# Kernel optimization log

Hardware: AMD Instinct MI355X
Metric: run time of the kernel (lower is better)

## Reference

```python
import jax, jax.numpy as jnp
import numpy as np

N = 50000
E = 800000
F_IN = 128
HID = 16
HEADS = 8
C = 16
NEG_SLOPE = 0.2


def setup_inputs() -> dict:
    key = jax.random.key(0)
    ks = jax.random.split(key, 12)
    glorot = lambda k, shape: jax.random.normal(k, shape, jnp.float32) * jnp.sqrt(2.0 / (shape[0] + shape[-1]))
    return {
        "x": jax.random.normal(ks[0], (N, F_IN), jnp.float32),
        "edge_index": jax.random.randint(ks[1], (2, E), 0, N, jnp.int32),
        "x2": jax.random.normal(ks[2], (N, F_IN), jnp.float32),
        "edge_index2": jax.random.randint(ks[3], (2, E), 0, N, jnp.int32),
        # conv1: GATConv(F_IN -> HID, heads=HEADS, concat=True)
        "W1": glorot(ks[4], (F_IN, HEADS * HID)),
        "a1_src": glorot(ks[5], (HEADS, HID)),
        "a1_dst": glorot(ks[6], (HEADS, HID)),
        "b1": jnp.zeros((HEADS * HID,), jnp.float32),
        # conv2: GATConv(HEADS*HID -> C, heads=1, concat=False)
        "W2": glorot(ks[7], (HEADS * HID, 1 * C)),
        "a2_src": glorot(ks[8], (1, C)),
        "a2_dst": glorot(ks[9], (1, C)),
        "b2": jnp.zeros((C,), jnp.float32),
    }


def gat_conv(x, edge_index, W, a_src, a_dst, bias, concat):
    """PyG-style GATConv with self-loops, segment softmax over destinations."""
    n = x.shape[0]
    heads, out = a_src.shape
    h = (x @ W).reshape(n, heads, out)               # [N, H, O]
    loops = jnp.arange(n, dtype=edge_index.dtype)
    src = jnp.concatenate([edge_index[0], loops])     # messages flow src -> dst
    dst = jnp.concatenate([edge_index[1], loops])
    alpha_s = jnp.einsum('nho,ho->nh', h, a_src)
    alpha_d = jnp.einsum('nho,ho->nh', h, a_dst)
    e = jax.nn.leaky_relu(alpha_s[src] + alpha_d[dst], NEG_SLOPE)  # [E+N, H]
    m = jax.lax.stop_gradient(jax.ops.segment_max(e, dst, num_segments=n))
    w = jnp.exp(e - m[dst])
    denom = jax.ops.segment_sum(w, dst, num_segments=n)
    alpha = w / (denom[dst] + 1e-16)                  # segment softmax
    msg = h[src] * alpha[:, :, None]                  # [E+N, H, O]
    agg = jax.ops.segment_sum(msg, dst, num_segments=n)
    agg = agg.reshape(n, heads * out) if concat else agg.mean(axis=1)
    return agg + bias


def forward_once(x, edge_index, W1, a1_src, a1_dst, b1, W2, a2_src, a2_dst, b2):
    # dropout(p=0.6) is identity in eval mode
    h = jax.nn.elu(gat_conv(x, edge_index, W1, a1_src, a1_dst, b1, concat=True))
    return gat_conv(h, edge_index, W2, a2_src, a2_dst, b2, concat=False)


def reference(x, edge_index, x2, edge_index2, W1, a1_src, a1_dst, b1, W2, a2_src, a2_dst, b2):
    y = forward_once(x, edge_index, W1, a1_src, a1_dst, b1, W2, a2_src, a2_dst, b2)
    z = forward_once(x2, edge_index2, W1, a1_src, a1_dst, b1, W2, a2_src, a2_dst, b2)
    eps = 1e-8
    ny = jnp.maximum(jnp.linalg.norm(y, axis=1), eps)
    nz = jnp.maximum(jnp.linalg.norm(z, axis=1), eps)
    cos = jnp.sum(y * z, axis=1) / (ny * nz)
    ls_y = jax.nn.log_softmax(y, axis=1)
    ls_z = jax.nn.log_softmax(z, axis=1)
    return (ls_y, 1.0 - cos, ls_z, ls_y, ls_y)
```

## Files before the change

kernel.cpp:

```cpp
#include <hip/hip_runtime.h>
#include <hip/hip_bf16.h>

#define N_NODES 50000
#define N_EDGES 800000
#define F_INS   128
#define HIDDEN  16
#define HEADS   8
#define HO      128
#define C_OUT   16
#define NEG_SLOPE 0.2f
#define SLOT    64
#define NB_G1   ((N_NODES + 63) / 64)
#define NB_GAT1 ((N_NODES + 3) / 4)
#define NB_G2   ((N_NODES + 16) / 16)

#define NP      50016
#define AS_ST   ((size_t)NP * 8)
#define H1B_ST  ((size_t)NP * 64)
#define HL1_ST  ((size_t)N_NODES * 64)
#define H2_ST   ((size_t)NP * 16)
#define AS2_ST  ((size_t)NP)

#define NCLS     128
#define CLS_MUL  1342u
#define CLS_SH   19
#define CAP      8192
#define CHUNK    2048
#define NB_BKT   ((N_EDGES + CHUNK - 1) / CHUNK)

typedef unsigned short u16;
typedef unsigned int   u32;
typedef int v4i __attribute__((ext_vector_type(4)));
typedef short bf16x8 __attribute__((ext_vector_type(8)));
typedef float f32x4 __attribute__((ext_vector_type(4)));

__device__ __forceinline__ float bf2f(u16 u) {
    union { u32 i; float f; } t; t.i = ((u32)u) << 16; return t.f;
}
__device__ __forceinline__ float bflo(u32 q) {
    union { u32 i; float f; } t; t.i = q << 16; return t.f;
}
__device__ __forceinline__ float bfhi(u32 q) {
    union { u32 i; float f; } t; t.i = q & 0xFFFF0000u; return t.f;
}
__device__ __forceinline__ u32 f2bf(float f) {
    union { float f; u32 i; } t; t.f = f;
    u32 x = t.i;
    u32 lsb = (x >> 16) & 1u;
    x += 0x7FFFu + lsb;
    return x >> 16;
}
__device__ __forceinline__ float lrelu(float t) {
    return fmaxf(t, NEG_SLOPE * t);
}
__device__ __forceinline__ int cls_of(int d) { return (int)(((u32)d * CLS_MUL) >> CLS_SH); }
__host__ __device__ __forceinline__ int cls_base(int c) { return (int)(((u32)c * 524288u + (CLS_MUL - 1)) / CLS_MUL); }

__global__ void k_wt(const float* __restrict__ W1, const float* __restrict__ a1s,
                     const float* __restrict__ a1d, u32* __restrict__ w1t,
                     u32* __restrict__ a1t) {
    int t = threadIdx.x;
    if (blockIdx.x < 32) {
        int e = blockIdx.x * 256 + t;
        int c = e >> 6, kp = e & 63;
        float lo = W1[(2 * kp) * 128 + c];
        float hi = W1[(2 * kp + 1) * 128 + c];
        w1t[e] = (f2bf(hi) << 16) | f2bf(lo);
    } else {
        #pragma unroll
        for (int i = 0; i < 4; ++i) {
            int wi = t + i * 256;
            int n = wi >> 6, kp = wi & 63;
            int h = n >> 1;
            const float* av = ((n & 1) ? a1d : a1s) + h * 16;
            float s0 = 0.f, s1 = 0.f;
            #pragma unroll
            for (int c = 0; c < 16; ++c) {
                s0 += W1[(2 * kp) * 128 + h * 16 + c] * av[c];
                s1 += W1[(2 * kp + 1) * 128 + h * 16 + c] * av[c];
            }
            a1t[wi] = (f2bf(s1) << 16) | f2bf(s0);
        }
    }
}

__launch_bounds__(256)
__global__ void k_bucket(const int* __restrict__ ei0, const int* __restrict__ ei1,
                         int* __restrict__ gcur, u32* __restrict__ bucket) {
    __shared__ int cnt[NCLS];
    __shared__ int base[NCLS];
    int t = threadIdx.x;
    int g = blockIdx.x & 1;
    int chunk = blockIdx.x >> 1;
    int e0 = chunk * CHUNK + t * 8;
    bool act = e0 < N_EDGES;

    if (t < NCLS) cnt[t] = 0;
    __syncthreads();

    const int* src = g ? ei1 : ei0;
    const int* dst = src + N_EDGES;
    int d8[8], s8[8], c8[8];
    if (act) {
        v4i da = *(const v4i*)(dst + e0), db = *(const v4i*)(dst + e0 + 4);
        v4i sa = *(const v4i*)(src + e0), sb = *(const v4i*)(src + e0 + 4);
        d8[0]=da[0]; d8[1]=da[1]; d8[2]=da[2]; d8[3]=da[3];
        d8[4]=db[0]; d8[5]=db[1]; d8[6]=db[2]; d8[7]=db[3];
        s8[0]=sa[0]; s8[1]=sa[1]; s8[2]=sa[2]; s8[3]=sa[3];
        s8[4]=sb[0]; s8[5]=sb[1]; s8[6]=sb[2]; s8[7]=sb[3];
        #pragma unroll
        for (int j = 0; j < 8; ++j) {
            c8[j] = cls_of(d8[j]);
            atomicAdd(&cnt[c8[j]], 1);
        }
    }
    __syncthreads();
    if (t < NCLS) {
        int n = cnt[t];
        base[t] = n ? atomicAdd(&gcur[g * NCLS + t], n) : 0;
        cnt[t] = 0;
    }
    __syncthreads();
    if (act) {
        #pragma unroll
        for (int j = 0; j < 8; ++j) {
            int c = c8[j];
            int p = atomicAdd(&cnt[c], 1);
            bucket[(size_t)(g * NCLS + c) * CAP + base[c] + p] =
                ((u32)d8[j] << 16) | (u32)s8[j];
        }
    }
}

__launch_bounds__(256)
__global__ void k_build(const int* __restrict__ gcur, const u32* __restrict__ bucket,
                        int* __restrict__ cursor, u16* __restrict__ col) {
    __shared__ int cnt[391];
    int t = threadIdx.x;
    int c = blockIdx.x & (NCLS - 1);
    int g = blockIdx.x >> 7;
    int d0 = cls_base(c);
    int d1 = (c == NCLS - 1) ? N_NODES : cls_base(c + 1);
    int nn = d1 - d0;
    for (int j = t; j < nn; j += 256) cnt[j] = 0;
    __syncthreads();

    int size = gcur[g * NCLS + c];
    const u32* bp = bucket + (size_t)(g * NCLS + c) * CAP;
    u16* cl = col + (size_t)g * N_NODES * SLOT;
    for (int i = t; i < size; i += 256) {
        u32 e = bp[i];
        int d = (int)(e >> 16);
        int s = (int)(e & 0xFFFFu);
        int p = atomicAdd(&cnt[d - d0], 1);
        if (p < SLOT) cl[(size_t)d * SLOT + p] = (u16)s;
    }
    __syncthreads();
    int* cur = cursor + g * N_NODES;
    for (int j = t; j < nn; j += 256) {
        int d = d0 + j;
        int raw = cnt[j];
        int n0 = min(raw, SLOT);
        int n1 = (n0 + 7) & ~7;
        u16* cw = cl + (size_t)d * SLOT;
        for (int p = n0; p < n1; ++p) cw[p] = (u16)N_NODES;
        cur[d] = raw;
    }
}

__launch_bounds__(256)
__global__ void k_gemm1(const float* __restrict__ x1g, const float* __restrict__ x2g,
                        const u32* __restrict__ w1t, const u32* __restrict__ a1t,
                        u32* __restrict__ h1b, float* __restrict__ as_,
                        float* __restrict__ ad_) {
    __shared__ u32 xls[4096];
    int t = threadIdx.x;
    int bid = blockIdx.x;
    int g = bid >= NB_G1;
    if (g) bid -= NB_G1;
    const float* x = g ? x2g : x1g;
    u32*   h1o = h1b + (size_t)g * H1B_ST;
    float* aso = as_ + (size_t)g * AS_ST;
    float* ado = ad_ + (size_t)g * AS_ST;
    int r0 = bid * 64;

    const float2* x2p = (const float2*)x;
    #pragma unroll
    for (int i = 0; i < 16; ++i) {
        int A = t + i * 256;
        int wi = A >> 10, kt = (A >> 8) & 3, L = (A >> 2) & 63, jj = A & 3;
        int m = L & 15, qd = L >> 4;
        int r = r0 + wi * 16 + m;
        int pp = kt * 16 + qd * 4 + jj;
        float2 v = make_float2(0.f, 0.f);
        if (r < N_NODES) v = x2p[(size_t)r * 64 + pp];
        xls[A] = (f2bf(v.y) << 16) | f2bf(v.x);
    }
    __syncthreads();

    int lane = t & 63;
    int wid = t >> 6;
    int n = lane & 15, quad = lane >> 4;

    f32x4 acc[8], acca;
    #pragma unroll
    for (int ct = 0; ct < 8; ++ct) acc[ct] = (f32x4){0.f, 0.f, 0.f, 0.f};
    acca = (f32x4){0.f, 0.f, 0.f, 0.f};

    #pragma unroll
    for (int kt = 0; kt < 4; ++kt) {
        union { uint4 u; bf16x8 v; } af;
        af.u = *(const uint4*)(xls + wid * 1024 + kt * 256 + lane * 4);
        #pragma unroll
        for (int ct = 0; ct < 8; ++ct) {
            union { uint4 u; bf16x8 v; } bf_;
            bf_.u = *(const uint4*)(w1t + (ct * 16 + n) * 64 + kt * 16 + quad * 4);
            acc[ct] = __builtin_amdgcn_mfma_f32_16x16x32_bf16(af.v, bf_.v, acc[ct], 0, 0, 0);
        }
        union { uint4 u; bf16x8 v; } ba;
        ba.u = *(const uint4*)(a1t + n * 64 + kt * 16 + quad * 4);
        acca = __builtin_amdgcn_mfma_f32_16x16x32_bf16(af.v, ba.v, acca, 0, 0, 0);
    }

    int h = n >> 1;
    #pragma unroll
    for (int reg = 0; reg < 4; ++reg) {
        int gr = r0 + wid * 16 + quad * 4 + reg;
        bool ok = gr <= N_NODES;
        float av = (gr == N_NODES) ? -1e30f : acca[reg];
        if (ok) {
            if (n & 1) ado[gr * 8 + h] = av;
            else       aso[gr * 8 + h] = av;
        }
        #pragma unroll
        for (int ct = 0; ct < 8; ++ct) {
            u32 my = f2bf(acc[ct][reg]);
            u32 ot = (u32)__shfl_xor((int)my, 1);
            if (!(n & 1) && ok)
                h1o[(size_t)gr * 64 + ct * 8 + (n >> 1)] = (ot << 16) | my;
        }
    }
}

__launch_bounds__(256)
__global__ void k_gat1(const u32* __restrict__ h1b, const float* __restrict__ as_,
                       const float* __restrict__ ad_, const int* __restrict__ cursor,
                       const u16* __restrict__ col, const float* __restrict__ b1,
                       u32* __restrict__ hL1) {
    int t = threadIdx.x;
    int lane = t & 63;
    int bid = blockIdx.x;
    int g = bid >= NB_GAT1;
    if (g) bid -= NB_GAT1;
    int node = bid * 4 + (t >> 6);

    const u32*   h1  = h1b + (size_t)g * H1B_ST;
    const float* as1 = as_ + (size_t)g * AS_ST;
    const float* ad1 = ad_ + (size_t)g * AS_ST;
    const u16*   cp  = col + ((size_t)g * N_NODES + node) * SLOT;

    int hc = lane >> 3;
    int ha = lane & 7;
    int j8 = lane >> 3;
    int vb = hc << 2;

    float ad_a = ad1[node * 8 + ha];
    float as_c = as1[node * 8 + hc];
    float ad_c = ad1[node * 8 + hc];

    float w = __expf(lrelu(as_c + ad_c));
    float denom = w;
    u32 q = h1[(u32)node * 64 + (u32)lane];
    float ax = w * bflo(q), ay = w * bfhi(q);

    int deg = min(cursor[g * N_NODES + node], SLOT);
    int nb = (deg + 7) >> 3;
    for (int b = 0; b < nb; ++b) {
        int e = b * 8;
        ushort4 sa4 = *(const ushort4*)(cp + e);
        ushort4 sb4 = *(const ushort4*)(cp + e + 4);
        u32 q0 = h1[((u32)sa4.x << 6) | (u32)lane];
        u32 q1 = h1[((u32)sa4.y << 6) | (u32)lane];
        u32 q2 = h1[((u32)sa4.z << 6) | (u32)lane];
        u32 q3 = h1[((u32)sa4.w << 6) | (u32)lane];
        u32 q4 = h1[((u32)sb4.x << 6) | (u32)lane];
        u32 q5 = h1[((u32)sb4.y << 6) | (u32)lane];
        u32 q6 = h1[((u32)sb4.z << 6) | (u32)lane];
        u32 q7 = h1[((u32)sb4.w << 6) | (u32)lane];

        int sA = cp[e + j8];
        float A = as1[sA * 8 + ha];
        int wli = __float_as_int(__expf(lrelu(A + ad_a)));
        float w0 = __int_as_float(__builtin_amdgcn_ds_bpermute(vb,       wli));
        float w1 = __int_as_float(__builtin_amdgcn_ds_bpermute(vb + 32,  wli));
        float w2 = __int_as_float(__builtin_amdgcn_ds_bpermute(vb + 64,  wli));
        float w3 = __int_as_float(__builtin_amdgcn_ds_bpermute(vb + 96,  wli));
        float w4 = __int_as_float(__builtin_amdgcn_ds_bpermute(vb + 128, wli));
        float w5 = __int_as_float(__builtin_amdgcn_ds_bpermute(vb + 160, wli));
        float w6 = __int_as_float(__builtin_amdgcn_ds_bpermute(vb + 192, wli));
        float w7 = __int_as_float(__builtin_amdgcn_ds_bpermute(vb + 224, wli));

        denom += ((w0 + w1) + (w2 + w3)) + ((w4 + w5) + (w6 + w7));
        ax += w0 * bflo(q0) + w1 * bflo(q1) + w2 * bflo(q2) + w3 * bflo(q3)
            + w4 * bflo(q4) + w5 * bflo(q5) + w6 * bflo(q6) + w7 * bflo(q7);
        ay += w0 * bfhi(q0) + w1 * bfhi(q1) + w2 * bfhi(q2) + w3 * bfhi(q3)
            + w4 * bfhi(q4) + w5 * bfhi(q5) + w6 * bfhi(q6) + w7 * bfhi(q7);
    }
    float inv = 1.f / (denom + 1e-16f);
    int c = lane * 2;
    float o0 = ax * inv + b1[c];
    float o1 = ay * inv + b1[c + 1];
    o0 = (o0 > 0.f) ? o0 : (__expf(o0) - 1.f);
    o1 = (o1 > 0.f) ? o1 : (__expf(o1) - 1.f);
    hL1[(size_t)g * HL1_ST + (size_t)node * 64 + lane] = (f2bf(o1) << 16) | f2bf(o0);
}

__launch_bounds__(256)
__global__ void k_gemm2(const u32* __restrict__ hL1, const float* __restrict__ W2,
                        const float* __restrict__ a2s, const float* __restrict__ a2d,
                        float* __restrict__ h2, float* __restrict__ as2,
                        float* __restrict__ ad2) {
    __shared__ float w2s[F_INS * C_OUT];
    __shared__ float hs[16 * 136];
    int t = threadIdx.x;
    int bid = blockIdx.x;
    int g = bid >= NB_G2;
    if (g) bid -= NB_G2;
    const u16* hL = (const u16*)(hL1 + (size_t)g * HL1_ST);
    float* h2o  = h2  + (size_t)g * H2_ST;
    float* as2o = as2 + (size_t)g * AS2_ST;
    float* ad2o = ad2 + (size_t)g * AS2_ST;

    const float4* w4 = (const float4*)W2;
    #pragma unroll
    for (int i = 0; i < 2; ++i) {
        int idx = t + i * 256;
        ((float4*)w2s)[idx] = w4[idx];
    }
    int r0 = bid * 16;
    const ushort4* hg = (const ushort4*)hL;
    #pragma unroll
    for (int i = 0; i < 2; ++i) {
        int idx = t + i * 256;
        int r  = idx >> 5;
        int c4 = idx & 31;
        ushort4 qq = make_ushort4(0, 0, 0, 0);
        if (r0 + r < N_NODES) qq = hg[(size_t)(r0 + r) * 32 + c4];
        float4 v; v.x = bf2f(qq.x); v.y = bf2f(qq.y); v.z = bf2f(qq.z); v.w = bf2f(qq.w);
        *(float4*)(hs + r * 136 + c4 * 4) = v;
    }
    __syncthreads();

    int c = t & 15, r = t >> 4;
    float acc = 0.f;
    #pragma unroll 8
    for (int k = 0; k < F_INS; ++k) acc += hs[r * 136 + k] * w2s[k * C_OUT + c];
    int n = r0 + r;
    if (n <= N_NODES) h2o[(size_t)n * C_OUT + c] = acc;

    float sa = acc * a2s[c];
    float sd = acc * a2d[c];
    #pragma unroll
    for (int m = 1; m < 16; m <<= 1) {
        sa += __shfl_xor(sa, m);
        sd += __shfl_xor(sd, m);
    }
    if (c == 0 && n <= N_NODES) {
        as2o[n] = (n == N_NODES) ? -1e30f : sa;
        ad2o[n] = sd;
    }
}

__device__ __forceinline__ float gat2_node(const float* __restrict__ h2g,
                                           const float* __restrict__ as2g,
                                           const float* __restrict__ ad2g,
                                           const int* __restrict__ curg,
                                           const u16* __restrict__ cp,
                                           const float* __restrict__ b2,
                                           int node, int c) {
    float ad = ad2g[node];
    float w = __expf(lrelu(as2g[node] + ad));
    float denom = w;
    float acc = w * h2g[(u32)node * C_OUT + (u32)c];

    int deg = min(curg[node], SLOT);
    int nb = (deg + 7) >> 3;
    for (int b = 0; b < nb; ++b) {
        const u16* ce = cp + b * 8;
        ushort4 sa4 = *(const ushort4*)ce;
        ushort4 sb4 = *(const ushort4*)(ce + 4);
        int s0 = sa4.x, s1 = sa4.y, s2 = sa4.z, s3 = sa4.w;
        int s4 = sb4.x, s5 = sb4.y, s6 = sb4.z, s7 = sb4.w;
        float A0 = as2g[s0], A1 = as2g[s1], A2 = as2g[s2], A3 = as2g[s3];
        float A4 = as2g[s4], A5 = as2g[s5], A6 = as2g[s6], A7 = as2g[s7];
        float v0 = h2g[(u32)(s0 * C_OUT + c)], v1 = h2g[(u32)(s1 * C_OUT + c)];
        float v2 = h2g[(u32)(s2 * C_OUT + c)], v3 = h2g[(u32)(s3 * C_OUT + c)];
        float v4 = h2g[(u32)(s4 * C_OUT + c)], v5 = h2g[(u32)(s5 * C_OUT + c)];
        float v6 = h2g[(u32)(s6 * C_OUT + c)], v7 = h2g[(u32)(s7 * C_OUT + c)];
        float w0 = __expf(lrelu(A0 + ad)), w1 = __expf(lrelu(A1 + ad));
        float w2 = __expf(lrelu(A2 + ad)), w3 = __expf(lrelu(A3 + ad));
        float w4 = __expf(lrelu(A4 + ad)), w5 = __expf(lrelu(A5 + ad));
        float w6 = __expf(lrelu(A6 + ad)), w7 = __expf(lrelu(A7 + ad));
        denom += ((w0 + w1) + (w2 + w3)) + ((w4 + w5) + (w6 + w7));
        acc += (w0 * v0 + w1 * v1 + w2 * v2 + w3 * v3)
             + (w4 * v4 + w5 * v5 + w6 * v6 + w7 * v7);
    }
    return acc / (denom + 1e-16f) + b2[c];
}

__launch_bounds__(256)
__global__ void k_gat2e(const float* __restrict__ h2, const float* __restrict__ as2,
                        const float* __restrict__ ad2, const int* __restrict__ cursor,
                        const u16* __restrict__ col, const float* __restrict__ b2,
                        float* __restrict__ out) {
    int t = threadIdx.x;
    int node = blockIdx.x * 16 + (t >> 4);
    int c = t & 15;

    float yv = gat2_node(h2, as2, ad2, cursor,
                         col + (size_t)node * SLOT, b2, node, c);
    float zv = gat2_node(h2 + H2_ST, as2 + AS2_ST, ad2 + AS2_ST, cursor + N_NODES,
                         col + ((size_t)N_NODES + node) * SLOT, b2, node, c);

    float my = yv, mz = zv;
    #pragma unroll
    for (int m = 1; m < 16; m <<= 1) {
        my = fmaxf(my, __shfl_xor(my, m));
        mz = fmaxf(mz, __shfl_xor(mz, m));
    }
    float sy = __expf(yv - my), sz = __expf(zv - mz);
    float dot = yv * zv, ny = yv * yv, nz = zv * zv;
    #pragma unroll
    for (int m = 1; m < 16; m <<= 1) {
        sy  += __shfl_xor(sy, m);
        sz  += __shfl_xor(sz, m);
        dot += __shfl_xor(dot, m);
        ny  += __shfl_xor(ny, m);
        nz  += __shfl_xor(nz, m);
    }
    float lsey = my + __logf(sy);
    float lsez = mz + __logf(sz);
    float omc = 1.f - dot / (fmaxf(sqrtf(ny), 1e-8f) * fmaxf(sqrtf(nz), 1e-8f));

    const int O1 = N_NODES * C_OUT;
    const int O2 = O1 + N_NODES;
    const int O3 = O2 + N_NODES * C_OUT;
    const int O4 = O3 + N_NODES * C_OUT;
    float ly = yv - lsey;
    float lz = zv - lsez;
    int base = node * 16 + c;
    out[base]      = ly;
    out[O2 + base] = lz;
    out[O3 + base] = ly;
    out[O4 + base] = ly;
    if (c == 0) out[O1 + node] = omc;
}

extern "C" void kernel_launch(void* const* d_in, const int* in_sizes, int n_in,
                              void* d_out, int out_size, void* d_ws, size_t ws_size,
                              hipStream_t stream) {
    (void)in_sizes; (void)n_in; (void)out_size; (void)ws_size;
    const float* x1  = (const float*)d_in[0];
    const int*   ei1 = (const int*)d_in[1];
    const float* x2  = (const float*)d_in[2];
    const int*   ei2 = (const int*)d_in[3];
    const float* W1  = (const float*)d_in[4];
    const float* a1s = (const float*)d_in[5];
    const float* a1d = (const float*)d_in[6];
    const float* b1  = (const float*)d_in[7];
    const float* W2  = (const float*)d_in[8];
    const float* a2s = (const float*)d_in[9];
    const float* a2d = (const float*)d_in[10];
    const float* b2  = (const float*)d_in[11];
    float* out = (float*)d_out;

    char* p = (char*)d_ws;
    int* gcur      = (int*)p; p += (size_t)2 * NCLS * 4;
    u32* w1t       = (u32*)p; p += (size_t)128 * 64 * 4;
    u32* a1t       = (u32*)p; p += (size_t)16 * 64 * 4;
    int* cursor    = (int*)p; p += (size_t)2 * N_NODES * 4;
    u16* col       = (u16*)p; p += (size_t)2 * N_NODES * SLOT * 2;
    float* as1  = (float*)p; p += (size_t)2 * AS_ST * 4;
    float* ad1  = (float*)p; p += (size_t)2 * AS_ST * 4;
    float* h2   = (float*)p; p += (size_t)2 * H2_ST * 4;
    float* as2  = (float*)p; p += (size_t)2 * AS2_ST * 4;
    float* ad2  = (float*)p; p += (size_t)2 * AS2_ST * 4;
    u32* hL1    = (u32*)p;   p += (size_t)2 * HL1_ST * 4;
    u32* h1b    = (u32*)p;   p += (size_t)2 * H1B_ST * 4;
    u32* bucket = h1b;

    hipMemsetAsync(gcur, 0, (size_t)2 * NCLS * 4, stream);
    k_wt    <<<33, 256, 0, stream>>>(W1, a1s, a1d, w1t, a1t);
    k_bucket<<<2 * NB_BKT, 256, 0, stream>>>(ei1, ei2, gcur, bucket);
    k_build <<<2 * NCLS, 256, 0, stream>>>(gcur, bucket, cursor, col);
    k_gemm1 <<<2 * NB_G1, 256, 0, stream>>>(x1, x2, w1t, a1t, h1b, as1, ad1);
    k_gat1  <<<2 * NB_GAT1, 256, 0, stream>>>(h1b, as1, ad1, cursor, col, b1, hL1);
    k_gemm2 <<<2 * NB_G2, 256, 0, stream>>>(hL1, W2, a2s, a2d, h2, as2, ad2);
    k_gat2e <<<N_NODES / 16, 256, 0, stream>>>(h2, as2, ad2, cursor, col, b2, out);
}
```

Baseline: 318.4 us.

## Software-pipeline GAT gathers, stage CSR build in LDS, use packed bf16 convert

The GAT1 and GAT2 aggregation loops become double-buffered: neighbour indices and feature gathers for the next block of 8 edges are issued before the current block is consumed. This hides gather latency at the cost of more registers. GAT2 now computes each edge weight once per lane and broadcasts it with ds_bpermute, instead of every channel lane recomputing all 8 exponentials. The CSR build stages column lists in LDS and writes them out with coalesced 16-byte stores. Manual bf16 rounding is replaced by the hardware v_cvt_pk_bf16_f32 instruction.

```diff
diff --git a/kernel.cpp b/kernel.cpp
--- a/kernel.cpp
+++ b/kernel.cpp
@@ -49,6 +49,11 @@
     u32 lsb = (x >> 16) & 1u;
     x += 0x7FFFu + lsb;
     return x >> 16;
+}
+__device__ __forceinline__ u32 cvtpk(float lo, float hi) {
+    u32 r;
+    asm("v_cvt_pk_bf16_f32 %0, %1, %2" : "=v"(r) : "v"(lo), "v"(hi));
+    return r;
 }
 __device__ __forceinline__ float lrelu(float t) {
     return fmaxf(t, NEG_SLOPE * t);
@@ -136,6 +141,7 @@
 __global__ void k_build(const int* __restrict__ gcur, const u32* __restrict__ bucket,
                         int* __restrict__ cursor, u16* __restrict__ col) {
     __shared__ int cnt[391];
+    __shared__ __align__(16) u16 scol[391 * SLOT];
     int t = threadIdx.x;
     int c = blockIdx.x & (NCLS - 1);
     int g = blockIdx.x >> 7;
@@ -147,25 +153,27 @@
 
     int size = gcur[g * NCLS + c];
     const u32* bp = bucket + (size_t)(g * NCLS + c) * CAP;
-    u16* cl = col + (size_t)g * N_NODES * SLOT;
     for (int i = t; i < size; i += 256) {
         u32 e = bp[i];
         int d = (int)(e >> 16);
         int s = (int)(e & 0xFFFFu);
         int p = atomicAdd(&cnt[d - d0], 1);
-        if (p < SLOT) cl[(size_t)d * SLOT + p] = (u16)s;
+        if (p < SLOT) scol[(d - d0) * SLOT + p] = (u16)s;
     }
     __syncthreads();
     int* cur = cursor + g * N_NODES;
     for (int j = t; j < nn; j += 256) {
-        int d = d0 + j;
         int raw = cnt[j];
         int n0 = min(raw, SLOT);
         int n1 = (n0 + 7) & ~7;
-        u16* cw = cl + (size_t)d * SLOT;
-        for (int p = n0; p < n1; ++p) cw[p] = (u16)N_NODES;
-        cur[d] = raw;
-    }
+        for (int p = n0; p < n1; ++p) scol[j * SLOT + p] = (u16)N_NODES;
+        cur[d0 + j] = raw;
+    }
+    __syncthreads();
+    uint4* dst = (uint4*)(col + ((size_t)g * N_NODES + d0) * SLOT);
+    const uint4* srcv = (const uint4*)scol;
+    int n16 = nn * 8;
+    for (int i = t; i < n16; i += 256) dst[i] = srcv[i];
 }
 
 __launch_bounds__(256)
@@ -194,7 +202,7 @@
         int pp = kt * 16 + qd * 4 + jj;
         float2 v = make_float2(0.f, 0.f);
         if (r < N_NODES) v = x2p[(size_t)r * 64 + pp];
-        xls[A] = (f2bf(v.y) << 16) | f2bf(v.x);
+        xls[A] = cvtpk(v.x, v.y);
     }
     __syncthreads();
 
@@ -234,13 +242,44 @@
         }
         #pragma unroll
         for (int ct = 0; ct < 8; ++ct) {
-            u32 my = f2bf(acc[ct][reg]);
-            u32 ot = (u32)__shfl_xor((int)my, 1);
+            float ot = __shfl_xor(acc[ct][reg], 1);
             if (!(n & 1) && ok)
-                h1o[(size_t)gr * 64 + ct * 8 + (n >> 1)] = (ot << 16) | my;
-        }
-    }
-}
+                h1o[(size_t)gr * 64 + ct * 8 + (n >> 1)] = cvtpk(acc[ct][reg], ot);
+        }
+    }
+}
+
+#define GAT1_ISSUE(I, q0,q1,q2,q3,q4,q5,q6,q7, A) do { \
+    u32 ix_=(I).x, iy_=(I).y, iz_=(I).z, iw_=(I).w; \
+    q0 = *(const u32*)(h1c + (((ix_ & 0xFFFFu) << 8) | lane4)); \
+    q1 = *(const u32*)(h1c + (((ix_ >> 16)     << 8) | lane4)); \
+    q2 = *(const u32*)(h1c + (((iy_ & 0xFFFFu) << 8) | lane4)); \
+    q3 = *(const u32*)(h1c + (((iy_ >> 16)     << 8) | lane4)); \
+    q4 = *(const u32*)(h1c + (((iz_ & 0xFFFFu) << 8) | lane4)); \
+    q5 = *(const u32*)(h1c + (((iz_ >> 16)     << 8) | lane4)); \
+    q6 = *(const u32*)(h1c + (((iw_ & 0xFFFFu) << 8) | lane4)); \
+    q7 = *(const u32*)(h1c + (((iw_ >> 16)     << 8) | lane4)); \
+    u32 ds_ = (j8 & 4) ? ((j8 & 2) ? iw_ : iz_) : ((j8 & 2) ? iy_ : ix_); \
+    u32 sA_ = (j8 & 1) ? (ds_ >> 16) : (ds_ & 0xFFFFu); \
+    A = *(const float*)(asc + ((sA_ << 5) | ha4)); \
+} while (0)
+
+#define GAT1_CONS(q0,q1,q2,q3,q4,q5,q6,q7, A) do { \
+    int wli_ = __float_as_int(__expf(lrelu((A) + ad_a))); \
+    float w0 = __int_as_float(__builtin_amdgcn_ds_bpermute(vb,       wli_)); \
+    float w1 = __int_as_float(__builtin_amdgcn_ds_bpermute(vb + 32,  wli_)); \
+    float w2 = __int_as_float(__builtin_amdgcn_ds_bpermute(vb + 64,  wli_)); \
+    float w3 = __int_as_float(__builtin_amdgcn_ds_bpermute(vb + 96,  wli_)); \
+    float w4 = __int_as_float(__builtin_amdgcn_ds_bpermute(vb + 128, wli_)); \
+    float w5 = __int_as_float(__builtin_amdgcn_ds_bpermute(vb + 160, wli_)); \
+    float w6 = __int_as_float(__builtin_amdgcn_ds_bpermute(vb + 192, wli_)); \
+    float w7 = __int_as_float(__builtin_amdgcn_ds_bpermute(vb + 224, wli_)); \
+    denom += ((w0 + w1) + (w2 + w3)) + ((w4 + w5) + (w6 + w7)); \
+    ax += w0 * bflo(q0) + w1 * bflo(q1) + w2 * bflo(q2) + w3 * bflo(q3) \
+        + w4 * bflo(q4) + w5 * bflo(q5) + w6 * bflo(q6) + w7 * bflo(q7); \
+    ay += w0 * bfhi(q0) + w1 * bfhi(q1) + w2 * bfhi(q2) + w3 * bfhi(q3) \
+        + w4 * bfhi(q4) + w5 * bfhi(q5) + w6 * bfhi(q6) + w7 * bfhi(q7); \
+} while (0)
 
 __launch_bounds__(256)
 __global__ void k_gat1(const u32* __restrict__ h1b, const float* __restrict__ as_,
@@ -254,8 +293,8 @@
     if (g) bid -= NB_GAT1;
     int node = bid * 4 + (t >> 6);
 
-    const u32*   h1  = h1b + (size_t)g * H1B_ST;
-    const float* as1 = as_ + (size_t)g * AS_ST;
+    const char*  h1c = (const char*)(h1b + (size_t)g * H1B_ST);
+    const char*  asc = (const char*)(as_ + (size_t)g * AS_ST);
     const float* ad1 = ad_ + (size_t)g * AS_ST;
     const u16*   cp  = col + ((size_t)g * N_NODES + node) * SLOT;
 
@@ -263,48 +302,46 @@
     int ha = lane & 7;
     int j8 = lane >> 3;
     int vb = hc << 2;
+    u32 lane4 = (u32)lane << 2;
+    u32 ha4 = (u32)ha << 2;
 
     float ad_a = ad1[node * 8 + ha];
-    float as_c = as1[node * 8 + hc];
+    float as_c = as_[(size_t)g * AS_ST + node * 8 + hc];
     float ad_c = ad1[node * 8 + hc];
 
     float w = __expf(lrelu(as_c + ad_c));
     float denom = w;
-    u32 q = h1[(u32)node * 64 + (u32)lane];
+    u32 q = *(const u32*)(h1c + (((u32)node << 8) | lane4));
     float ax = w * bflo(q), ay = w * bfhi(q);
 
     int deg = min(cursor[g * N_NODES + node], SLOT);
     int nb = (deg + 7) >> 3;
-    for (int b = 0; b < nb; ++b) {
-        int e = b * 8;
-        ushort4 sa4 = *(const ushort4*)(cp + e);
-        ushort4 sb4 = *(const ushort4*)(cp + e + 4);
-        u32 q0 = h1[((u32)sa4.x << 6) | (u32)lane];
-        u32 q1 = h1[((u32)sa4.y << 6) | (u32)lane];
-        u32 q2 = h1[((u32)sa4.z << 6) | (u32)lane];
-        u32 q3 = h1[((u32)sa4.w << 6) | (u32)lane];
-        u32 q4 = h1[((u32)sb4.x << 6) | (u32)lane];
-        u32 q5 = h1[((u32)sb4.y << 6) | (u32)lane];
-        u32 q6 = h1[((u32)sb4.z << 6) | (u32)lane];
-        u32 q7 = h1[((u32)sb4.w << 6) | (u32)lane];
-
-        int sA = cp[e + j8];
-        float A = as1[sA * 8 + ha];
-        int wli = __float_as_int(__expf(lrelu(A + ad_a)));
-        float w0 = __int_as_float(__builtin_amdgcn_ds_bpermute(vb,       wli));
-        float w1 = __int_as_float(__builtin_amdgcn_ds_bpermute(vb + 32,  wli));
-        float w2 = __int_as_float(__builtin_amdgcn_ds_bpermute(vb + 64,  wli));
-        float w3 = __int_as_float(__builtin_amdgcn_ds_bpermute(vb + 96,  wli));
-        float w4 = __int_as_float(__builtin_amdgcn_ds_bpermute(vb + 128, wli));
-        float w5 = __int_as_float(__builtin_amdgcn_ds_bpermute(vb + 160, wli));
-        float w6 = __int_as_float(__builtin_amdgcn_ds_bpermute(vb + 192, wli));
-        float w7 = __int_as_float(__builtin_amdgcn_ds_bpermute(vb + 224, wli));
-
-        denom += ((w0 + w1) + (w2 + w3)) + ((w4 + w5) + (w6 + w7));
-        ax += w0 * bflo(q0) + w1 * bflo(q1) + w2 * bflo(q2) + w3 * bflo(q3)
-            + w4 * bflo(q4) + w5 * bflo(q5) + w6 * bflo(q6) + w7 * bflo(q7);
-        ay += w0 * bfhi(q0) + w1 * bfhi(q1) + w2 * bfhi(q2) + w3 * bfhi(q3)
-            + w4 * bfhi(q4) + w5 * bfhi(q5) + w6 * bfhi(q6) + w7 * bfhi(q7);
+    if (nb) {
+        u32 qa0,qa1,qa2,qa3,qa4,qa5,qa6,qa7;
+        u32 qb0,qb1,qb2,qb3,qb4,qb5,qb6,qb7;
+        float Aa, Ab;
+        uint4 Ia, Ib;
+        Ia = *(const uint4*)cp;
+        GAT1_ISSUE(Ia, qa0,qa1,qa2,qa3,qa4,qa5,qa6,qa7, Aa);
+        if (nb > 1) {
+            Ib = *(const uint4*)(cp + 8);
+            GAT1_ISSUE(Ib, qb0,qb1,qb2,qb3,qb4,qb5,qb6,qb7, Ab);
+        }
+        int b = 0;
+        for (;;) {
+            GAT1_CONS(qa0,qa1,qa2,qa3,qa4,qa5,qa6,qa7, Aa);
+            if (++b >= nb) break;
+            if (b + 1 < nb) {
+                Ia = *(const uint4*)(cp + (b + 1) * 8);
+                GAT1_ISSUE(Ia, qa0,qa1,qa2,qa3,qa4,qa5,qa6,qa7, Aa);
+            }
+            GAT1_CONS(qb0,qb1,qb2,qb3,qb4,qb5,qb6,qb7, Ab);
+            if (++b >= nb) break;
+            if (b + 1 < nb) {
+                Ib = *(const uint4*)(cp + (b + 1) * 8);
+                GAT1_ISSUE(Ib, qb0,qb1,qb2,qb3,qb4,qb5,qb6,qb7, Ab);
+            }
+        }
     }
     float inv = 1.f / (denom + 1e-16f);
     int c = lane * 2;
@@ -312,7 +349,7 @@
     float o1 = ay * inv + b1[c + 1];
     o0 = (o0 > 0.f) ? o0 : (__expf(o0) - 1.f);
     o1 = (o1 > 0.f) ? o1 : (__expf(o1) - 1.f);
-    hL1[(size_t)g * HL1_ST + (size_t)node * 64 + lane] = (f2bf(o1) << 16) | f2bf(o0);
+    hL1[(size_t)g * HL1_ST + (size_t)node * 64 + lane] = cvtpk(o0, o1);
 }
 
 __launch_bounds__(256)
@@ -371,41 +408,74 @@
     }
 }
 
-__device__ __forceinline__ float gat2_node(const float* __restrict__ h2g,
-                                           const float* __restrict__ as2g,
-                                           const float* __restrict__ ad2g,
-                                           const int* __restrict__ curg,
-                                           const u16* __restrict__ cp,
-                                           const float* __restrict__ b2,
-                                           int node, int c) {
+#define GAT2_ISSUE(I, v0,v1,v2,v3,v4,v5,v6,v7, A) do { \
+    u32 ix_=(I).x, iy_=(I).y, iz_=(I).z, iw_=(I).w; \
+    v0 = *(const float*)(h2c + (((ix_ & 0xFFFFu) << 6) | c4)); \
+    v1 = *(const float*)(h2c + (((ix_ >> 16)     << 6) | c4)); \
+    v2 = *(const float*)(h2c + (((iy_ & 0xFFFFu) << 6) | c4)); \
+    v3 = *(const float*)(h2c + (((iy_ >> 16)     << 6) | c4)); \
+    v4 = *(const float*)(h2c + (((iz_ & 0xFFFFu) << 6) | c4)); \
+    v5 = *(const float*)(h2c + (((iz_ >> 16)     << 6) | c4)); \
+    v6 = *(const float*)(h2c + (((iw_ & 0xFFFFu) << 6) | c4)); \
+    v7 = *(const float*)(h2c + (((iw_ >> 16)     << 6) | c4)); \
+    u32 ds_ = (jsel & 4) ? ((jsel & 2) ? iw_ : iz_) : ((jsel & 2) ? iy_ : ix_); \
+    u32 sA_ = (jsel & 1) ? (ds_ >> 16) : (ds_ & 0xFFFFu); \
+    A = *(const float*)(as2c + (sA_ << 2)); \
+} while (0)
+
+#define GAT2_CONS(v0,v1,v2,v3,v4,v5,v6,v7, A) do { \
+    int wli_ = __float_as_int(__expf(lrelu((A) + ad))); \
+    float w0 = __int_as_float(__builtin_amdgcn_ds_bpermute(gb,      wli_)); \
+    float w1 = __int_as_float(__builtin_amdgcn_ds_bpermute(gb + 4,  wli_)); \
+    float w2 = __int_as_float(__builtin_amdgcn_ds_bpermute(gb + 8,  wli_)); \
+    float w3 = __int_as_float(__builtin_amdgcn_ds_bpermute(gb + 12, wli_)); \
+    float w4 = __int_as_float(__builtin_amdgcn_ds_bpermute(gb + 16, wli_)); \
+    float w5 = __int_as_float(__builtin_amdgcn_ds_bpermute(gb + 20, wli_)); \
+    float w6 = __int_as_float(__builtin_amdgcn_ds_bpermute(gb + 24, wli_)); \
+    float w7 = __int_as_float(__builtin_amdgcn_ds_bpermute(gb + 28, wli_)); \
+    denom += ((w0 + w1) + (w2 + w3)) + ((w4 + w5) + (w6 + w7)); \
+    acc += (w0 * v0 + w1 * v1 + w2 * v2 + w3 * v3) \
+         + (w4 * v4 + w5 * v5 + w6 * v6 + w7 * v7); \
+} while (0)
+
+__device__ __forceinline__ float gat2_node(const char* h2c, const char* as2c,
+                                           const float* __restrict__ ad2g, int deg,
+                                           const u16* __restrict__ cp, int node,
+                                           u32 c4, int jsel, u32 gb, float b2c) {
     float ad = ad2g[node];
-    float w = __expf(lrelu(as2g[node] + ad));
+    float w = __expf(lrelu(*(const float*)(as2c + ((u32)node << 2)) + ad));
     float denom = w;
-    float acc = w * h2g[(u32)node * C_OUT + (u32)c];
-
-    int deg = min(curg[node], SLOT);
+    float acc = w * *(const float*)(h2c + (((u32)node << 6) | c4));
+
     int nb = (deg + 7) >> 3;
-    for (int b = 0; b < nb; ++b) {
-        const u16* ce = cp + b * 8;
-        ushort4 sa4 = *(const ushort4*)ce;
-        ushort4 sb4 = *(const ushort4*)(ce + 4);
-        int s0 = sa4.x, s1 = sa4.y, s2 = sa4.z, s3 = sa4.w;
-        int s4 = sb4.x, s5 = sb4.y, s6 = sb4.z, s7 = sb4.w;
-        float A0 = as2g[s0], A1 = as2g[s1], A2 = as2g[s2], A3 = as2g[s3];
-        float A4 = as2g[s4], A5 = as2g[s5], A6 = as2g[s6], A7 = as2g[s7];
-        float v0 = h2g[(u32)(s0 * C_OUT + c)], v1 = h2g[(u32)(s1 * C_OUT + c)];
-        float v2 = h2g[(u32)(s2 * C_OUT + c)], v3 = h2g[(u32)(s3 * C_OUT + c)];
-        float v4 = h2g[(u32)(s4 * C_OUT + c)], v5 = h2g[(u32)(s5 * C_OUT + c)];
-        float v6 = h2g[(u32)(s6 * C_OUT + c)], v7 = h2g[(u32)(s7 * C_OUT + c)];
-        float w0 = __expf(lrelu(A0 + ad)), w1 = __expf(lrelu(A1 + ad));
-        float w2 = __expf(lrelu(A2 + ad)), w3 = __expf(lrelu(A3 + ad));
-        float w4 = __expf(lrelu(A4 + ad)), w5 = __expf(lrelu(A5 + ad));
-        float w6 = __expf(lrelu(A6 + ad)), w7 = __expf(lrelu(A7 + ad));
-        denom += ((w0 + w1) + (w2 + w3)) + ((w4 + w5) + (w6 + w7));
-        acc += (w0 * v0 + w1 * v1 + w2 * v2 + w3 * v3)
-             + (w4 * v4 + w5 * v5 + w6 * v6 + w7 * v7);
-    }
-    return acc / (denom + 1e-16f) + b2[c];
+    if (nb) {
+        float va0,va1,va2,va3,va4,va5,va6,va7;
+        float vc0,vc1,vc2,vc3,vc4,vc5,vc6,vc7;
+        float Aa, Ac;
+        uint4 Ia, Ic;
+        Ia = *(const uint4*)cp;
+        GAT2_ISSUE(Ia, va0,va1,va2,va3,va4,va5,va6,va7, Aa);
+        if (nb > 1) {
+            Ic = *(const uint4*)(cp + 8);
+            GAT2_ISSUE(Ic, vc0,vc1,vc2,vc3,vc4,vc5,vc6,vc7, Ac);
+        }
+        int b = 0;
+        for (;;) {
+            GAT2_CONS(va0,va1,va2,va3,va4,va5,va6,va7, Aa);
+            if (++b >= nb) break;
+            if (b + 1 < nb) {
+                Ia = *(const uint4*)(cp + (b + 1) * 8);
+                GAT2_ISSUE(Ia, va0,va1,va2,va3,va4,va5,va6,va7, Aa);
+            }
+            GAT2_CONS(vc0,vc1,vc2,vc3,vc4,vc5,vc6,vc7, Ac);
+            if (++b >= nb) break;
+            if (b + 1 < nb) {
+                Ic = *(const uint4*)(cp + (b + 1) * 8);
+                GAT2_ISSUE(Ic, vc0,vc1,vc2,vc3,vc4,vc5,vc6,vc7, Ac);
+            }
+        }
+    }
+    return acc / (denom + 1e-16f) + b2c;
 }
 
 __launch_bounds__(256)
@@ -416,11 +486,19 @@
     int t = threadIdx.x;
     int node = blockIdx.x * 16 + (t >> 4);
     int c = t & 15;
-
-    float yv = gat2_node(h2, as2, ad2, cursor,
-                         col + (size_t)node * SLOT, b2, node, c);
-    float zv = gat2_node(h2 + H2_ST, as2 + AS2_ST, ad2 + AS2_ST, cursor + N_NODES,
-                         col + ((size_t)N_NODES + node) * SLOT, b2, node, c);
+    int lane = t & 63;
+    u32 c4 = (u32)c << 2;
+    int jsel = lane & 7;
+    u32 gb = (u32)(lane & 48) << 2;
+    float b2c = b2[c];
+
+    int degY = min(cursor[node], SLOT);
+    int degZ = min(cursor[N_NODES + node], SLOT);
+    float yv = gat2_node((const char*)h2, (const char*)as2, ad2, degY,
+                         col + (size_t)node * SLOT, node, c4, jsel, gb, b2c);
+    float zv = gat2_node((const char*)(h2 + H2_ST), (const char*)(as2 + AS2_ST),
+                         ad2 + AS2_ST, degZ,
+                         col + ((size_t)N_NODES + node) * SLOT, node, c4, jsel, gb, b2c);
 
     float my = yv, mz = zv;
     #pragma unroll
```

Measured after the change: 315.6 us. Within noise of the previous version (-0.9%).
